# Kernel tuning notes

Measured on AMD Instinct MI355X. Metric: run time of the kernel, lower is better.

## Reference

```python
import jax, jax.numpy as jnp
import numpy as np


def setup_inputs() -> dict:
    key = jax.random.key(0)
    ks = jax.random.split(key, 8)
    B, T, C = 4, 1024, 1024
    s = 1.0 / np.sqrt(C)
    return {
        "q": jax.random.normal(ks[0], (B, T, C), jnp.float32),
        "k": jax.random.normal(ks[1], (B, T, C), jnp.float32),
        "v": jax.random.normal(ks[2], (B, T, C), jnp.float32),
        "Wq": jax.random.normal(ks[3], (C, C), jnp.float32) * s,
        "Wk": jax.random.normal(ks[4], (C, C), jnp.float32) * s,
        "Wv": jax.random.normal(ks[5], (C, C), jnp.float32) * s,
        "Wp": jax.random.normal(ks[6], (C, C), jnp.float32) * s,
        "bp": jnp.zeros((C,), jnp.float32),
        "n_head": 16,
        "kernel_size": 16,
    }


def reference(q, k, v, Wq, Wk, Wv, Wp, bp, n_head, kernel_size):
    B, T, C = q.shape
    H = n_head
    D = C // H

    def split_heads(x, W):
        # nn.Linear applies x @ W.T
        return (x @ W.T).reshape(B, T, H, D).transpose(0, 2, 1, 3)  # (B,H,T,D)

    qp = split_heads(q, Wq)
    kp = split_heads(k, Wk)
    vp = split_heads(v, Wv)

    # Faithful to the torch double loop: wei[b,h,i,j] = sum over feature dims
    # d in [max(0, j-ks), min(T, j+ks)) (clipped to [0,D)) of qp[b,h,i,d]*kp[b,h,i,d] / sqrt(D).
    # Both windows index sequence position i; the window slides over the head_dim axis.
    p = qp * kp / jnp.sqrt(jnp.asarray(D, qp.dtype))          # (B,H,T,D)
    cs = jnp.cumsum(p, axis=-1)
    cs = jnp.concatenate([jnp.zeros(cs.shape[:-1] + (1,), cs.dtype), cs], axis=-1)  # (B,H,T,D+1)
    j = jnp.arange(T)
    start = jnp.clip(j - kernel_size, 0, D)                   # (T,)
    end = jnp.clip(jnp.minimum(j + kernel_size, T), 0, D)     # (T,)
    wei = cs[..., end] - cs[..., start]                       # (B,H,T,T): windowed partial dot of row i

    attn = jax.nn.softmax(wei, axis=-1)
    out = jnp.einsum("bhts,bhsd->bhtd", attn, vp)             # (B,H,T,D)
    out = out.transpose(0, 2, 1, 3).reshape(B, T, C)
    out = out @ Wp.T + bp
    # dropout is identity in eval mode
    return out
```

## Files before the change

### kernel.cpp

```cpp
#include <hip/hip_runtime.h>
#include <hip/hip_bf16.h>
#include <stdint.h>


typedef __bf16 bf16x8 __attribute__((ext_vector_type(8)));
typedef float f32x4 __attribute__((ext_vector_type(4)));

#define AS1(p) ((__attribute__((address_space(1))) void*)(p))
#define AS3(p) ((__attribute__((address_space(3))) void*)(p))

__global__ __launch_bounds__(256) void cvt_kernel(
    const float* __restrict__ q, const float* __restrict__ k,
    const float* __restrict__ v, const float* __restrict__ Wq,
    const float* __restrict__ Wk, const float* __restrict__ Wv,
    const float* __restrict__ Wp,
    ushort4* __restrict__ qkv_bf, ushort4* __restrict__ w_bf,
    float* __restrict__ tails)
{
  if (blockIdx.x == 16384) {
    float4* tz = (float4*)tails;
    tz[threadIdx.x * 4 + 0] = make_float4(0.f, 0.f, 0.f, 0.f);
    tz[threadIdx.x * 4 + 1] = make_float4(0.f, 0.f, 0.f, 0.f);
    tz[threadIdx.x * 4 + 2] = make_float4(0.f, 0.f, 0.f, 0.f);
    tz[threadIdx.x * 4 + 3] = make_float4(0.f, 0.f, 0.f, 0.f);
    return;
  }
  int idx = blockIdx.x * 256 + threadIdx.x;
  const float* src; ushort4* dst; int i;
  if (idx < 3145728) {
    int which = idx >> 20; i = idx & 1048575;
    src = which == 0 ? q : which == 1 ? k : v;
    dst = qkv_bf + (size_t)which * 1048576 + i;
  } else {
    int w = idx - 3145728; int which = w >> 18; i = w & 262143;
    src = which == 0 ? Wq : which == 1 ? Wk : which == 2 ? Wv : Wp;
    dst = w_bf + w;
  }
  float4 val = ((const float4*)src)[i];
  union { ushort4 u; __hip_bfloat16 h[4]; } c;
  c.h[0] = __float2bfloat16(val.x); c.h[1] = __float2bfloat16(val.y);
  c.h[2] = __float2bfloat16(val.z); c.h[3] = __float2bfloat16(val.w);
  dst[0] = c.u;
}

__device__ __forceinline__ void gemm_tile128(
    const __hip_bfloat16* __restrict__ A, const __hip_bfloat16* __restrict__ Bw,
    __hip_bfloat16* __restrict__ C, float* tailAtomic, int rowInB)
{
  const int N = 1024, K = 1024;
  __shared__ __align__(16) __hip_bfloat16 As[2][128 * 32];
  __shared__ __align__(16) __hip_bfloat16 Bs[2][128 * 32];
  const int t = threadIdx.x;
  const int wv = t >> 6, lane = t & 63;
  const int wRow = (wv >> 1) * 64, wCol = (wv & 1) * 64;
  const int mrow = lane & 15, kq = lane >> 4;

  f32x4 acc[4][4] = {};

  for (int k0 = 0; k0 < K; k0 += 64) {
    __syncthreads();
#pragma unroll
    for (int half = 0; half < 2; ++half)
#pragma unroll
      for (int tI = 0; tI < 2; ++tI) {
        int chunk = wv * 2 + tI;
        int byteOff = chunk * 1024 + lane * 16;
        int row = byteOff >> 6;
        int colEl = (byteOff & 63) >> 1;
        const __hip_bfloat16* ga = A + (size_t)row * K + k0 + half * 32 + colEl;
        __builtin_amdgcn_global_load_lds(AS1((void*)ga), AS3(&As[half][chunk * 512]), 16, 0, 0);
        const __hip_bfloat16* gb = Bw + (size_t)row * K + k0 + half * 32 + colEl;
        __builtin_amdgcn_global_load_lds(AS1((void*)gb), AS3(&Bs[half][chunk * 512]), 16, 0, 0);
      }
    __syncthreads();

#pragma unroll
    for (int half = 0; half < 2; ++half) {
      bf16x8 af[4], bf[4];
#pragma unroll
      for (int mi = 0; mi < 4; ++mi)
        af[mi] = *(const bf16x8*)&As[half][(wRow + mi * 16 + mrow) * 32 + kq * 8];
#pragma unroll
      for (int ni = 0; ni < 4; ++ni)
        bf[ni] = *(const bf16x8*)&Bs[half][(wCol + ni * 16 + mrow) * 32 + kq * 8];
#pragma unroll
      for (int mi = 0; mi < 4; ++mi)
#pragma unroll
        for (int ni = 0; ni < 4; ++ni)
          acc[mi][ni] = __builtin_amdgcn_mfma_f32_16x16x32_bf16(af[mi], bf[ni], acc[mi][ni], 0, 0, 0);
    }
  }

#pragma unroll
  for (int mi = 0; mi < 4; ++mi)
#pragma unroll
    for (int ni = 0; ni < 4; ++ni)
#pragma unroll
      for (int r = 0; r < 4; ++r) {
        int row = wRow + mi * 16 + kq * 4 + r;
        int col = wCol + ni * 16 + mrow;
        C[(size_t)row * N + col] = __float2bfloat16(acc[mi][ni][r]);
      }

  if (tailAtomic) {
#pragma unroll
    for (int ni = 0; ni < 4; ++ni) {
      float s = 0.0f;
#pragma unroll
      for (int mi = 0; mi < 4; ++mi)
#pragma unroll
        for (int r = 0; r < 4; ++r) {
          int localRow = rowInB + wRow + mi * 16 + kq * 4 + r;
          if (localRow >= 80) s += acc[mi][ni][r];
        }
      s += __shfl_xor(s, 16, 64);
      s += __shfl_xor(s, 32, 64);
      if (kq == 0) atomicAdd(&tailAtomic[wCol + ni * 16 + mrow], s);
    }
  }
}

__global__ __launch_bounds__(256) void qkv_gemm_kernel(
    const __hip_bfloat16* __restrict__ QKVbf, const __hip_bfloat16* __restrict__ Wbf,
    __hip_bfloat16* __restrict__ QKVp, float* __restrict__ tails)
{
  int l = blockIdx.x;
  int n = l / 96, mm = l % 96, z = mm >> 5, m = mm & 31;
  float* tailAtomic = nullptr;
  int rowInB = (m & 7) * 128;
  if (z == 2) tailAtomic = tails + (size_t)(m >> 3) * 1024 + n * 128;
  gemm_tile128(
      QKVbf + (size_t)z * 4194304 + (size_t)m * 131072,
      Wbf + (size_t)z * 1048576 + (size_t)n * 131072,
      QKVp + (size_t)z * 4194304 + (size_t)m * 131072 + n * 128,
      tailAtomic, rowInB);
}

__global__ __launch_bounds__(256) void final_gemm_kernel(
    const __hip_bfloat16* __restrict__ Abf, const __hip_bfloat16* __restrict__ Wpbf,
    float* __restrict__ Out, const float* __restrict__ biasAll)
{
  const int N = 1024, K = 1024;
  int l = blockIdx.x;
  int m = l & 63, n = l >> 6;
  const __hip_bfloat16* A = Abf + (size_t)m * 65536;
  const __hip_bfloat16* Bw = Wpbf + (size_t)n * 65536;
  float* C = Out + (size_t)m * 65536 + n * 64;
  const float* bias = biasAll + n * 64;

  __shared__ __align__(16) __hip_bfloat16 As[2][64 * 32];
  __shared__ __align__(16) __hip_bfloat16 Bs[2][64 * 32];
  const int t = threadIdx.x;
  const int wv = t >> 6, lane = t & 63;
  const int wRow = (wv >> 1) * 32, wCol = (wv & 1) * 32;
  const int mrow = lane & 15, kq = lane >> 4;

  f32x4 acc[2][2] = {};

  for (int k0 = 0; k0 < K; k0 += 64) {
    __syncthreads();
#pragma unroll
    for (int tI = 0; tI < 4; ++tI) {
      int c = wv * 4 + tI;
      int half, ch;
      const __hip_bfloat16* gsrc;
      __hip_bfloat16* ldst;
      if (c < 8) { half = c >> 2; ch = c & 3;
        int byteOff = ch * 1024 + lane * 16;
        gsrc = A + (size_t)(byteOff >> 6) * K + k0 + half * 32 + ((byteOff & 63) >> 1);
        ldst = &As[half][ch * 512];
      } else { int cb = c - 8; half = cb >> 2; ch = cb & 3;
        int byteOff = ch * 1024 + lane * 16;
        gsrc = Bw + (size_t)(byteOff >> 6) * K + k0 + half * 32 + ((byteOff & 63) >> 1);
        ldst = &Bs[half][ch * 512];
      }
      __builtin_amdgcn_global_load_lds(AS1((void*)gsrc), AS3(ldst), 16, 0, 0);
    }
    __syncthreads();

#pragma unroll
    for (int half = 0; half < 2; ++half) {
      bf16x8 af[2], bf[2];
#pragma unroll
      for (int mi = 0; mi < 2; ++mi)
        af[mi] = *(const bf16x8*)&As[half][(wRow + mi * 16 + mrow) * 32 + kq * 8];
#pragma unroll
      for (int ni = 0; ni < 2; ++ni)
        bf[ni] = *(const bf16x8*)&Bs[half][(wCol + ni * 16 + mrow) * 32 + kq * 8];
#pragma unroll
      for (int mi = 0; mi < 2; ++mi)
#pragma unroll
        for (int ni = 0; ni < 2; ++ni)
          acc[mi][ni] = __builtin_amdgcn_mfma_f32_16x16x32_bf16(af[mi], bf[ni], acc[mi][ni], 0, 0, 0);
    }
  }

#pragma unroll
  for (int mi = 0; mi < 2; ++mi)
#pragma unroll
    for (int ni = 0; ni < 2; ++ni)
#pragma unroll
      for (int r = 0; r < 4; ++r) {
        int row = wRow + mi * 16 + kq * 4 + r;
        int col = wCol + ni * 16 + mrow;
        __builtin_nontemporal_store(acc[mi][ni][r] + bias[col],
                                    &C[(size_t)row * N + col]);
      }
}

__global__ __launch_bounds__(256) void attn_kernel(
    const __hip_bfloat16* __restrict__ QP, const __hip_bfloat16* __restrict__ KP,
    const __hip_bfloat16* __restrict__ VP, const float* __restrict__ tails,
    __hip_bfloat16* __restrict__ OUTA)
{
  const int b = blockIdx.z, h = blockIdx.y, i0 = blockIdx.x * 64;
  const int t = threadIdx.x, lane = t & 63, wv = t >> 6;

  __shared__ __align__(16) char bufA[64 * 68 * 4];
  float (*csl)[68] = (float(*)[68])bufA;
  __hip_bfloat16 (*vpt)[104] = (__hip_bfloat16(*)[104])bufA;
  __shared__ __align__(16) __hip_bfloat16 wlb[64][96];
  __shared__ float scl[64], tlw[64], tail[64];

  if (t < 64) tail[t] = tails[(size_t)b * 1024 + h * 64 + t];

  {
    const int i = t >> 2, seg = t & 3;
    const size_t base = ((size_t)(b * 1024 + i0 + i)) * 1024 + h * 64 + seg * 16;
    bf16x8 q0 = *(const bf16x8*)(QP + base);
    bf16x8 q1 = *(const bf16x8*)(QP + base + 8);
    bf16x8 k0 = *(const bf16x8*)(KP + base);
    bf16x8 k1 = *(const bf16x8*)(KP + base + 8);
    float cs[16];
    float run = 0.0f;
#pragma unroll
    for (int x = 0; x < 8; ++x) {
      run += (float)q0[x] * (float)k0[x] * 0.125f;
      cs[x] = run;
    }
#pragma unroll
    for (int x = 0; x < 8; ++x) {
      run += (float)q1[x] * (float)k1[x] * 0.125f;
      cs[8 + x] = run;
    }
    float t1 = __shfl_up(run, 1, 4);
    float t2 = __shfl_up(run, 2, 4);
    float t3 = __shfl_up(run, 3, 4);
    float off = 0.0f;
    if (seg > 0) off += t1;
    if (seg > 1) off += t2;
    if (seg > 2) off += t3;
    float4* dst = (float4*)&csl[i][seg * 16];
#pragma unroll
    for (int x4 = 0; x4 < 4; ++x4)
      dst[x4] = make_float4(cs[4 * x4] + off, cs[4 * x4 + 1] + off,
                            cs[4 * x4 + 2] + off, cs[4 * x4 + 3] + off);
  }
  __syncthreads();

  {
    int i = t >> 2, jg = t & 3;
    float wloc[20];
    float mx = 0.0f;
#pragma unroll
    for (int q = 0; q < 20; ++q) {
      int j = jg + 4 * q;
      int s = j - 16; s = s < 0 ? 0 : s;
      int e = j + 16; e = e > 64 ? 64 : e;
      float w = csl[i][e - 1] - (s > 0 ? csl[i][s - 1] : 0.0f);
      wloc[q] = w;
      mx = fmaxf(mx, w);
    }
    mx = fmaxf(mx, __shfl_xor(mx, 1, 64));
    mx = fmaxf(mx, __shfl_xor(mx, 2, 64));
    float sum = 0.0f;
#pragma unroll
    for (int q = 0; q < 20; ++q) {
      float e_ = __expf(wloc[q] - mx);
      wlb[i][jg + 4 * q] = __float2bfloat16(e_);
      sum += e_;
    }
#pragma unroll
    for (int q = 0; q < 4; ++q)
      wlb[i][80 + jg + 4 * q] = __float2bfloat16(0.0f);
    sum += __shfl_xor(sum, 1, 64);
    sum += __shfl_xor(sum, 2, 64);
    float tw = __expf(-mx);
    sum += 944.0f * tw;
    if (jg == 0) { scl[i] = 1.0f / sum; tlw[i] = tw / sum; }
  }
  __syncthreads();

  for (int idx = t; idx < 80 * 64; idx += 256) {
    int j = idx >> 6, d = idx & 63;
    vpt[d][j] = VP[((size_t)(b * 1024 + j)) * 1024 + h * 64 + d];
  }
  for (int idx = t; idx < 64 * 16; idx += 256) {
    int d = idx >> 4, j = 80 + (idx & 15);
    vpt[d][j] = __float2bfloat16(0.0f);
  }
  __syncthreads();

  {
    const int mh = (wv >> 1) * 32, nh = (wv & 1) * 32;
    const int mrow = lane & 15, kq = lane >> 4;
    f32x4 acc[2][2] = {};
#pragma unroll
    for (int k0 = 0; k0 < 96; k0 += 32) {
      bf16x8 af[2], bf[2];
#pragma unroll
      for (int mi = 0; mi < 2; ++mi)
        af[mi] = *(const bf16x8*)&wlb[mh + mi * 16 + mrow][k0 + kq * 8];
#pragma unroll
      for (int ni = 0; ni < 2; ++ni)
        bf[ni] = *(const bf16x8*)&vpt[nh + ni * 16 + mrow][k0 + kq * 8];
#pragma unroll
      for (int mi = 0; mi < 2; ++mi)
#pragma unroll
        for (int ni = 0; ni < 2; ++ni)
          acc[mi][ni] = __builtin_amdgcn_mfma_f32_16x16x32_bf16(af[mi], bf[ni], acc[mi][ni], 0, 0, 0);
    }
#pragma unroll
    for (int mi = 0; mi < 2; ++mi)
#pragma unroll
      for (int ni = 0; ni < 2; ++ni)
#pragma unroll
        for (int r = 0; r < 4; ++r) {
          int i = mh + mi * 16 + kq * 4 + r;
          int d = nh + ni * 16 + mrow;
          float o = acc[mi][ni][r] * scl[i] + tlw[i] * tail[d];
          OUTA[((size_t)(b * 1024 + i0 + i)) * 1024 + h * 64 + d] = __float2bfloat16(o);
        }
  }
}

extern "C" void kernel_launch(void* const* d_in, const int* in_sizes, int n_in,
                              void* d_out, int out_size, void* d_ws, size_t ws_size,
                              hipStream_t stream)
{
  (void)in_sizes; (void)n_in; (void)out_size; (void)ws_size;
  const float* q  = (const float*)d_in[0];
  const float* k  = (const float*)d_in[1];
  const float* v  = (const float*)d_in[2];
  const float* Wq = (const float*)d_in[3];
  const float* Wk = (const float*)d_in[4];
  const float* Wv = (const float*)d_in[5];
  const float* Wp = (const float*)d_in[6];
  const float* bp = (const float*)d_in[7];

  char* ws = (char*)d_ws;
  __hip_bfloat16* qkv_bf = (__hip_bfloat16*)(ws);
  __hip_bfloat16* w_bf   = (__hip_bfloat16*)(ws + 25165824);
  __hip_bfloat16* QKVp   = (__hip_bfloat16*)(ws + 33554432);
  __hip_bfloat16* OUTA   = (__hip_bfloat16*)(ws + 58720256);
  float*          tails  = (float*)(ws + 67108864);
  float* out = (float*)d_out;

  cvt_kernel<<<dim3(16385), 256, 0, stream>>>(q, k, v, Wq, Wk, Wv, Wp,
      (ushort4*)qkv_bf, (ushort4*)w_bf, tails);
  qkv_gemm_kernel<<<dim3(768), 256, 0, stream>>>(qkv_bf, w_bf, QKVp, tails);
  attn_kernel<<<dim3(16, 16, 4), 256, 0, stream>>>(QKVp, QKVp + (size_t)4194304,
                                                   QKVp + (size_t)2 * 4194304, tails, OUTA);
  final_gemm_kernel<<<dim3(1024), 256, 0, stream>>>(OUTA, w_bf + (size_t)3 * 1048576,
                                                    out, bp);
}
```

Measured before the change: 179.4 us.

## Compute V tail sums algebraically and skip projecting unused V rows

The V projection GEMM now computes only the first 128 rows of each batch (the rows attention reads individually). The tail sum over rows at or above 80 is obtained by summing raw V rows first and then multiplying by Wv in two small kernels, instead of reducing projected rows with atomics. This removes most of the V projection GEMM work. The final projection GEMM tile also grows from 64x64 to 128x64 for more reuse per block. In exchange it adds two small serial launches, and accumulating before the projection changes the bf16 rounding.

```diff
diff --git a/kernel.cpp b/kernel.cpp
--- a/kernel.cpp
+++ b/kernel.cpp
@@ -8,6 +8,10 @@
 
 #define AS1(p) ((__attribute__((address_space(1))) void*)(p))
 #define AS3(p) ((__attribute__((address_space(3))) void*)(p))
+
+__device__ __forceinline__ float b2f(unsigned short h) {
+  union { unsigned int u; float f; } x; x.u = ((unsigned int)h) << 16; return x.f;
+}
 
 __global__ __launch_bounds__(256) void cvt_kernel(
     const float* __restrict__ q, const float* __restrict__ k,
@@ -15,10 +19,10 @@
     const float* __restrict__ Wk, const float* __restrict__ Wv,
     const float* __restrict__ Wp,
     ushort4* __restrict__ qkv_bf, ushort4* __restrict__ w_bf,
-    float* __restrict__ tails)
+    float* __restrict__ vsum)
 {
   if (blockIdx.x == 16384) {
-    float4* tz = (float4*)tails;
+    float4* tz = (float4*)vsum;
     tz[threadIdx.x * 4 + 0] = make_float4(0.f, 0.f, 0.f, 0.f);
     tz[threadIdx.x * 4 + 1] = make_float4(0.f, 0.f, 0.f, 0.f);
     tz[threadIdx.x * 4 + 2] = make_float4(0.f, 0.f, 0.f, 0.f);
@@ -43,9 +47,41 @@
   dst[0] = c.u;
 }
 
+__global__ __launch_bounds__(256) void vsum_kernel(
+    const __hip_bfloat16* __restrict__ Vbf, float* __restrict__ vsum)
+{
+  int b = blockIdx.x >> 3, rc = blockIdx.x & 7;
+  int c0 = threadIdx.x * 4;
+  int j0 = 80 + rc * 118;
+  float s0 = 0.f, s1 = 0.f, s2 = 0.f, s3 = 0.f;
+  for (int jj = 0; jj < 118; ++jj) {
+    ushort4 u = *(const ushort4*)(Vbf + ((size_t)(b * 1024 + j0 + jj)) * 1024 + c0);
+    s0 += b2f(u.x); s1 += b2f(u.y); s2 += b2f(u.z); s3 += b2f(u.w);
+  }
+  float* dst = vsum + b * 1024 + c0;
+  atomicAdd(dst + 0, s0); atomicAdd(dst + 1, s1);
+  atomicAdd(dst + 2, s2); atomicAdd(dst + 3, s3);
+}
+
+__global__ __launch_bounds__(256) void tails_kernel(
+    const __hip_bfloat16* __restrict__ Wvbf, const float* __restrict__ vsum,
+    float* __restrict__ tails)
+{
+  int b = blockIdx.x >> 2;
+  int c = ((blockIdx.x & 3) << 8) + threadIdx.x;
+  const float* vs = vsum + b * 1024;
+  float acc = 0.f;
+  for (int k0 = 0; k0 < 1024; k0 += 8) {
+    bf16x8 w = *(const bf16x8*)(Wvbf + (size_t)c * 1024 + k0);
+#pragma unroll
+    for (int x = 0; x < 8; ++x) acc += vs[k0 + x] * (float)w[x];
+  }
+  tails[b * 1024 + c] = acc;
+}
+
 __device__ __forceinline__ void gemm_tile128(
     const __hip_bfloat16* __restrict__ A, const __hip_bfloat16* __restrict__ Bw,
-    __hip_bfloat16* __restrict__ C, float* tailAtomic, int rowInB)
+    __hip_bfloat16* __restrict__ C)
 {
   const int N = 1024, K = 1024;
   __shared__ __align__(16) __hip_bfloat16 As[2][128 * 32];
@@ -101,39 +137,22 @@
         int col = wCol + ni * 16 + mrow;
         C[(size_t)row * N + col] = __float2bfloat16(acc[mi][ni][r]);
       }
-
-  if (tailAtomic) {
-#pragma unroll
-    for (int ni = 0; ni < 4; ++ni) {
-      float s = 0.0f;
-#pragma unroll
-      for (int mi = 0; mi < 4; ++mi)
-#pragma unroll
-        for (int r = 0; r < 4; ++r) {
-          int localRow = rowInB + wRow + mi * 16 + kq * 4 + r;
-          if (localRow >= 80) s += acc[mi][ni][r];
-        }
-      s += __shfl_xor(s, 16, 64);
-      s += __shfl_xor(s, 32, 64);
-      if (kq == 0) atomicAdd(&tailAtomic[wCol + ni * 16 + mrow], s);
-    }
-  }
 }
 
 __global__ __launch_bounds__(256) void qkv_gemm_kernel(
     const __hip_bfloat16* __restrict__ QKVbf, const __hip_bfloat16* __restrict__ Wbf,
-    __hip_bfloat16* __restrict__ QKVp, float* __restrict__ tails)
+    __hip_bfloat16* __restrict__ QKVp)
 {
   int l = blockIdx.x;
-  int n = l / 96, mm = l % 96, z = mm >> 5, m = mm & 31;
-  float* tailAtomic = nullptr;
-  int rowInB = (m & 7) * 128;
-  if (z == 2) tailAtomic = tails + (size_t)(m >> 3) * 1024 + n * 128;
+  int n = l / 68, r = l % 68;
+  int z, m;
+  if (r < 32)      { z = 0; m = r; }
+  else if (r < 64) { z = 1; m = r - 32; }
+  else             { z = 2; m = (r - 64) * 8; }
   gemm_tile128(
       QKVbf + (size_t)z * 4194304 + (size_t)m * 131072,
       Wbf + (size_t)z * 1048576 + (size_t)n * 131072,
-      QKVp + (size_t)z * 4194304 + (size_t)m * 131072 + n * 128,
-      tailAtomic, rowInB);
+      QKVp + (size_t)z * 4194304 + (size_t)m * 131072 + n * 128);
 }
 
 __global__ __launch_bounds__(256) void final_gemm_kernel(
@@ -142,34 +161,35 @@
 {
   const int N = 1024, K = 1024;
   int l = blockIdx.x;
-  int m = l & 63, n = l >> 6;
-  const __hip_bfloat16* A = Abf + (size_t)m * 65536;
+  int m = l & 31, n = l >> 5;
+  const __hip_bfloat16* A = Abf + (size_t)m * 131072;
   const __hip_bfloat16* Bw = Wpbf + (size_t)n * 65536;
-  float* C = Out + (size_t)m * 65536 + n * 64;
+  float* C = Out + (size_t)m * 131072 + n * 64;
   const float* bias = biasAll + n * 64;
 
-  __shared__ __align__(16) __hip_bfloat16 As[2][64 * 32];
+  __shared__ __align__(16) __hip_bfloat16 As[2][128 * 32];
   __shared__ __align__(16) __hip_bfloat16 Bs[2][64 * 32];
   const int t = threadIdx.x;
   const int wv = t >> 6, lane = t & 63;
-  const int wRow = (wv >> 1) * 32, wCol = (wv & 1) * 32;
+  const int wRow = (wv >> 1) * 64, wCol = (wv & 1) * 32;
   const int mrow = lane & 15, kq = lane >> 4;
 
-  f32x4 acc[2][2] = {};
+  f32x4 acc[4][2] = {};
 
   for (int k0 = 0; k0 < K; k0 += 64) {
     __syncthreads();
 #pragma unroll
-    for (int tI = 0; tI < 4; ++tI) {
-      int c = wv * 4 + tI;
-      int half, ch;
+    for (int tI = 0; tI < 6; ++tI) {
+      int c = wv * 6 + tI;
       const __hip_bfloat16* gsrc;
       __hip_bfloat16* ldst;
-      if (c < 8) { half = c >> 2; ch = c & 3;
+      if (c < 16) {
+        int half = c >> 3, ch = c & 7;
         int byteOff = ch * 1024 + lane * 16;
         gsrc = A + (size_t)(byteOff >> 6) * K + k0 + half * 32 + ((byteOff & 63) >> 1);
         ldst = &As[half][ch * 512];
-      } else { int cb = c - 8; half = cb >> 2; ch = cb & 3;
+      } else {
+        int cb = c - 16; int half = cb >> 2, ch = cb & 3;
         int byteOff = ch * 1024 + lane * 16;
         gsrc = Bw + (size_t)(byteOff >> 6) * K + k0 + half * 32 + ((byteOff & 63) >> 1);
         ldst = &Bs[half][ch * 512];
@@ -180,15 +200,15 @@
 
 #pragma unroll
     for (int half = 0; half < 2; ++half) {
-      bf16x8 af[2], bf[2];
-#pragma unroll
-      for (int mi = 0; mi < 2; ++mi)
+      bf16x8 af[4], bf[2];
+#pragma unroll
+      for (int mi = 0; mi < 4; ++mi)
         af[mi] = *(const bf16x8*)&As[half][(wRow + mi * 16 + mrow) * 32 + kq * 8];
 #pragma unroll
       for (int ni = 0; ni < 2; ++ni)
         bf[ni] = *(const bf16x8*)&Bs[half][(wCol + ni * 16 + mrow) * 32 + kq * 8];
 #pragma unroll
-      for (int mi = 0; mi < 2; ++mi)
+      for (int mi = 0; mi < 4; ++mi)
 #pragma unroll
         for (int ni = 0; ni < 2; ++ni)
           acc[mi][ni] = __builtin_amdgcn_mfma_f32_16x16x32_bf16(af[mi], bf[ni], acc[mi][ni], 0, 0, 0);
@@ -196,7 +216,7 @@
   }
 
 #pragma unroll
-  for (int mi = 0; mi < 2; ++mi)
+  for (int mi = 0; mi < 4; ++mi)
 #pragma unroll
     for (int ni = 0; ni < 2; ++ni)
 #pragma unroll
@@ -354,13 +374,16 @@
   __hip_bfloat16* QKVp   = (__hip_bfloat16*)(ws + 33554432);
   __hip_bfloat16* OUTA   = (__hip_bfloat16*)(ws + 58720256);
   float*          tails  = (float*)(ws + 67108864);
+  float*          vsum   = (float*)(ws + 67108864 + 16384);
   float* out = (float*)d_out;
 
   cvt_kernel<<<dim3(16385), 256, 0, stream>>>(q, k, v, Wq, Wk, Wv, Wp,
-      (ushort4*)qkv_bf, (ushort4*)w_bf, tails);
-  qkv_gemm_kernel<<<dim3(768), 256, 0, stream>>>(qkv_bf, w_bf, QKVp, tails);
+      (ushort4*)qkv_bf, (ushort4*)w_bf, vsum);
+  vsum_kernel<<<dim3(32), 256, 0, stream>>>(qkv_bf + (size_t)2 * 4194304, vsum);
+  tails_kernel<<<dim3(16), 256, 0, stream>>>(w_bf + (size_t)2 * 1048576, vsum, tails);
+  qkv_gemm_kernel<<<dim3(544), 256, 0, stream>>>(qkv_bf, w_bf, QKVp);
   attn_kernel<<<dim3(16, 16, 4), 256, 0, stream>>>(QKVp, QKVp + (size_t)4194304,
                                                    QKVp + (size_t)2 * 4194304, tails, OUTA);
-  final_gemm_kernel<<<dim3(1024), 256, 0, stream>>>(OUTA, w_bf + (size_t)3 * 1048576,
-                                                    out, bp);
-}
+  final_gemm_kernel<<<dim3(512), 256, 0, stream>>>(OUTA, w_bf + (size_t)3 * 1048576,
+                                                   out, bp);
+}
```

Measured after the change: 222.6 us. +24.1%, slower.
